# Kernel tuning notes

Hardware: AMD Instinct MI355X
Metric: run time of the kernel (lower is better)

Reference implementation:

```python
import jax, jax.numpy as jnp
import numpy as np

D_MODEL = 1024
N_OCTAVES = 3


def _index_maps(d_model: int, n_octaves: int):
    """Static octave index maps, matching HarmonicMixing._build_index_maps."""
    maps = []
    for octave in range(1, n_octaves + 1):
        stride = 2 ** octave
        up_src = np.arange(d_model // stride)
        up_tgt = up_src * stride                      # i -> i*stride
        down_src = np.arange(stride, d_model)
        down_tgt = down_src // stride                 # i -> i // stride (many-to-one)
        maps.append((up_src, up_tgt, down_src, down_tgt))
    return maps


def setup_inputs() -> dict:
    key = jax.random.key(0)
    k1, k2, k3 = jax.random.split(key, 3)
    x = jax.random.normal(k1, (8, 4096, D_MODEL), dtype=jnp.float32)
    up_weights = jax.random.uniform(k2, (N_OCTAVES,), dtype=jnp.float32)
    down_weights = jax.random.uniform(k3, (N_OCTAVES,), dtype=jnp.float32)
    return {"x": x, "up_weights": up_weights, "down_weights": down_weights}


def reference(x, up_weights, down_weights):
    d_model = x.shape[-1]
    maps = _index_maps(d_model, N_OCTAVES)
    out = x
    for o, (up_src, up_tgt, down_src, down_tgt) in enumerate(maps):
        up_w = jax.nn.sigmoid(up_weights[o])
        down_w = jax.nn.sigmoid(down_weights[o])
        # gather -> scale -> scatter-add (duplicate targets accumulate)
        out = out.at[..., up_tgt].add(up_w * x[..., up_src])
        out = out.at[..., down_tgt].add(down_w * x[..., down_src])
    return out
```

## Files before the change

### kernel.cpp

```cpp
#include <hip/hip_runtime.h>


constexpr int D = 1024;

using f4 = __attribute__((ext_vector_type(4))) float;

__global__ __launch_bounds__(256, 7) void harmonic_kernel(
    const float* __restrict__ x,
    const float* __restrict__ uwp,
    const float* __restrict__ dwp,
    float* __restrict__ out,
    const int n_rows)
{
    __shared__ float rowlo[4][512];
    __shared__ float S1lds[4][512];
    __shared__ float S2lds[4][256];

    const int t = threadIdx.x;
    const int w = t >> 6;
    const int l = t & 63;

    const float uw0 = 1.f / (1.f + __expf(-uwp[0]));
    const float uw1 = 1.f / (1.f + __expf(-uwp[1]));
    const float uw2 = 1.f / (1.f + __expf(-uwp[2]));
    const float dw0 = 1.f / (1.f + __expf(-dwp[0]));
    const float dw1 = 1.f / (1.f + __expf(-dwp[1]));
    const float dw2 = 1.f / (1.f + __expf(-dwp[2]));

    float* const RL = rowlo[w];
    float* const P1 = S1lds[w];
    float* const P2 = S2lds[w];

    auto loadrow = [&](f4* v, const float* p) {
#pragma unroll
        for (int m = 0; m < 4; ++m)
            v[m] = __builtin_nontemporal_load(reinterpret_cast<const f4*>(p + 256 * m));
    };

    auto process = [&](f4* v, float* po) {
        *reinterpret_cast<f4*>(&RL[4 * l])       = v[0];
        *reinterpret_cast<f4*>(&RL[256 + 4 * l]) = v[1];
#pragma unroll
        for (int m = 0; m < 4; ++m) {
            const float s1a = v[m].x + v[m].y;
            const float s1b = v[m].z + v[m].w;
            *reinterpret_cast<float2*>(&P1[128 * m + 2 * l]) = make_float2(s1a, s1b);
            P2[64 * m + l] = s1a + s1b;
        }

#pragma unroll
        for (int m = 0; m < 4; ++m) {
            const float2 u = *reinterpret_cast<const float2*>(&RL[128 * m + 2 * l]);
            v[m].x += uw0 * u.x;
            v[m].z += uw0 * u.y;
            v[m].x += uw1 * RL[64 * m + l];
            if ((l & 1) == 0) v[m].x += uw2 * RL[32 * m + (l >> 1)];
        }

#pragma unroll
        for (int m = 0; m < 2; ++m) {
            const f4 a = *reinterpret_cast<const f4*>(&P1[256 * m + 4 * l]);
            if (m > 0 || l > 0) v[m].x += dw0 * a.x;
            v[m].y += dw0 * a.y;
            v[m].z += dw0 * a.z;
            v[m].w += dw0 * a.w;
        }
        {
            const f4 b = *reinterpret_cast<const f4*>(&P2[4 * l]);
            if (l > 0) v[0].x += dw1 * b.x;
            v[0].y += dw1 * b.y;
            v[0].z += dw1 * b.z;
            v[0].w += dw1 * b.w;
        }
        if (l < 32) {
            const f4 p = *reinterpret_cast<const f4*>(&P2[8 * l]);
            const f4 q = *reinterpret_cast<const f4*>(&P2[8 * l + 4]);
            if (l > 0) v[0].x += dw2 * (p.x + p.y);
            v[0].y += dw2 * (p.z + p.w);
            v[0].z += dw2 * (q.x + q.y);
            v[0].w += dw2 * (q.z + q.w);
        }

#pragma unroll
        for (int m = 0; m < 4; ++m)
            __builtin_nontemporal_store(v[m], reinterpret_cast<f4*>(po + 256 * m));
    };

    const long long rowstep = 4LL * gridDim.x;
    long long row = 4LL * blockIdx.x + w;
    if (row >= n_rows) return;

    f4 vA[4], vB[4];
    loadrow(vA, x + row * D + 4 * l);
    for (;;) {
        const long long rowB = row + rowstep;
        const bool hasB = rowB < n_rows;
        if (hasB) loadrow(vB, x + rowB * D + 4 * l);
        process(vA, out + row * D + 4 * l);
        if (!hasB) return;

        const long long rowC = rowB + rowstep;
        const bool hasC = rowC < n_rows;
        if (hasC) loadrow(vA, x + rowC * D + 4 * l);
        process(vB, out + rowB * D + 4 * l);
        if (!hasC) return;
        row = rowC;
    }
}

extern "C" void kernel_launch(void* const* d_in, const int* in_sizes, int n_in,
                              void* d_out, int out_size, void* d_ws, size_t ws_size,
                              hipStream_t stream) {
    const float* x   = (const float*)d_in[0];
    const float* uwp = (const float*)d_in[1];
    const float* dwp = (const float*)d_in[2];
    float* out = (float*)d_out;
    const int n_rows = in_sizes[0] / D;
    int ngroups = (n_rows + 3) / 4;
    int nb = ngroups < 1792 ? ngroups : 1792;
    harmonic_kernel<<<nb, 256, 0, stream>>>(x, uwp, dwp, out, n_rows);
}
```

Measured before the change: 243.6 us.

## Replace persistent double-buffered grid-stride loop with one-row-per-wave launch

Drops the persistent kernel that software-pipelined row loads across a grid-stride loop and launches one block per four rows, so each wave handles exactly one row. This removes the loop overhead and the extra registers needed for the two row buffers, and relies on hardware wave scheduling to overlap memory latency instead of explicit prefetch. The cost is many more blocks (8192 for the test shape), each recomputing the six sigmoid weights and paying block launch overhead.

```diff
diff --git a/kernel.cpp b/kernel.cpp
--- a/kernel.cpp
+++ b/kernel.cpp
@@ -5,7 +5,7 @@
 
 using f4 = __attribute__((ext_vector_type(4))) float;
 
-__global__ __launch_bounds__(256, 7) void harmonic_kernel(
+__global__ __launch_bounds__(256) void harmonic_kernel(
     const float* __restrict__ x,
     const float* __restrict__ uwp,
     const float* __restrict__ dwp,
@@ -20,6 +20,9 @@
     const int w = t >> 6;
     const int l = t & 63;
 
+    const long long row = 4LL * blockIdx.x + w;
+    if (row >= n_rows) return;
+
     const float uw0 = 1.f / (1.f + __expf(-uwp[0]));
     const float uw1 = 1.f / (1.f + __expf(-uwp[1]));
     const float uw2 = 1.f / (1.f + __expf(-uwp[2]));
@@ -31,81 +34,60 @@
     float* const P1 = S1lds[w];
     float* const P2 = S2lds[w];
 
-    auto loadrow = [&](f4* v, const float* p) {
+    const float* px = x + row * D + 4 * l;
+    float*       po = out + row * D + 4 * l;
+
+    f4 v[4];
 #pragma unroll
-        for (int m = 0; m < 4; ++m)
-            v[m] = __builtin_nontemporal_load(reinterpret_cast<const f4*>(p + 256 * m));
-    };
+    for (int m = 0; m < 4; ++m)
+        v[m] = __builtin_nontemporal_load(reinterpret_cast<const f4*>(px + 256 * m));
 
-    auto process = [&](f4* v, float* po) {
-        *reinterpret_cast<f4*>(&RL[4 * l])       = v[0];
-        *reinterpret_cast<f4*>(&RL[256 + 4 * l]) = v[1];
+    *reinterpret_cast<f4*>(&RL[4 * l])       = v[0];
+    *reinterpret_cast<f4*>(&RL[256 + 4 * l]) = v[1];
 #pragma unroll
-        for (int m = 0; m < 4; ++m) {
-            const float s1a = v[m].x + v[m].y;
-            const float s1b = v[m].z + v[m].w;
-            *reinterpret_cast<float2*>(&P1[128 * m + 2 * l]) = make_float2(s1a, s1b);
-            P2[64 * m + l] = s1a + s1b;
-        }
+    for (int m = 0; m < 4; ++m) {
+        const float s1a = v[m].x + v[m].y;
+        const float s1b = v[m].z + v[m].w;
+        *reinterpret_cast<float2*>(&P1[128 * m + 2 * l]) = make_float2(s1a, s1b);
+        P2[64 * m + l] = s1a + s1b;
+    }
 
 #pragma unroll
-        for (int m = 0; m < 4; ++m) {
-            const float2 u = *reinterpret_cast<const float2*>(&RL[128 * m + 2 * l]);
-            v[m].x += uw0 * u.x;
-            v[m].z += uw0 * u.y;
-            v[m].x += uw1 * RL[64 * m + l];
-            if ((l & 1) == 0) v[m].x += uw2 * RL[32 * m + (l >> 1)];
-        }
+    for (int m = 0; m < 4; ++m) {
+        const float2 u = *reinterpret_cast<const float2*>(&RL[128 * m + 2 * l]);
+        v[m].x += uw0 * u.x;
+        v[m].z += uw0 * u.y;
+        v[m].x += uw1 * RL[64 * m + l];
+        if ((l & 1) == 0) v[m].x += uw2 * RL[32 * m + (l >> 1)];
+    }
 
 #pragma unroll
-        for (int m = 0; m < 2; ++m) {
-            const f4 a = *reinterpret_cast<const f4*>(&P1[256 * m + 4 * l]);
-            if (m > 0 || l > 0) v[m].x += dw0 * a.x;
-            v[m].y += dw0 * a.y;
-            v[m].z += dw0 * a.z;
-            v[m].w += dw0 * a.w;
-        }
-        {
-            const f4 b = *reinterpret_cast<const f4*>(&P2[4 * l]);
-            if (l > 0) v[0].x += dw1 * b.x;
-            v[0].y += dw1 * b.y;
-            v[0].z += dw1 * b.z;
-            v[0].w += dw1 * b.w;
-        }
-        if (l < 32) {
-            const f4 p = *reinterpret_cast<const f4*>(&P2[8 * l]);
-            const f4 q = *reinterpret_cast<const f4*>(&P2[8 * l + 4]);
-            if (l > 0) v[0].x += dw2 * (p.x + p.y);
-            v[0].y += dw2 * (p.z + p.w);
-            v[0].z += dw2 * (q.x + q.y);
-            v[0].w += dw2 * (q.z + q.w);
-        }
+    for (int m = 0; m < 2; ++m) {
+        const f4 a = *reinterpret_cast<const f4*>(&P1[256 * m + 4 * l]);
+        if (m > 0 || l > 0) v[m].x += dw0 * a.x;
+        v[m].y += dw0 * a.y;
+        v[m].z += dw0 * a.z;
+        v[m].w += dw0 * a.w;
+    }
+    {
+        const f4 b = *reinterpret_cast<const f4*>(&P2[4 * l]);
+        if (l > 0) v[0].x += dw1 * b.x;
+        v[0].y += dw1 * b.y;
+        v[0].z += dw1 * b.z;
+        v[0].w += dw1 * b.w;
+    }
+    if (l < 32) {
+        const f4 p = *reinterpret_cast<const f4*>(&P2[8 * l]);
+        const f4 q = *reinterpret_cast<const f4*>(&P2[8 * l + 4]);
+        if (l > 0) v[0].x += dw2 * (p.x + p.y);
+        v[0].y += dw2 * (p.z + p.w);
+        v[0].z += dw2 * (q.x + q.y);
+        v[0].w += dw2 * (q.z + q.w);
+    }
 
 #pragma unroll
-        for (int m = 0; m < 4; ++m)
-            __builtin_nontemporal_store(v[m], reinterpret_cast<f4*>(po + 256 * m));
-    };
-
-    const long long rowstep = 4LL * gridDim.x;
-    long long row = 4LL * blockIdx.x + w;
-    if (row >= n_rows) return;
-
-    f4 vA[4], vB[4];
-    loadrow(vA, x + row * D + 4 * l);
-    for (;;) {
-        const long long rowB = row + rowstep;
-        const bool hasB = rowB < n_rows;
-        if (hasB) loadrow(vB, x + rowB * D + 4 * l);
-        process(vA, out + row * D + 4 * l);
-        if (!hasB) return;
-
-        const long long rowC = rowB + rowstep;
-        const bool hasC = rowC < n_rows;
-        if (hasC) loadrow(vA, x + rowC * D + 4 * l);
-        process(vB, out + rowB * D + 4 * l);
-        if (!hasC) return;
-        row = rowC;
-    }
+    for (int m = 0; m < 4; ++m)
+        __builtin_nontemporal_store(v[m], reinterpret_cast<f4*>(po + 256 * m));
 }
 
 extern "C" void kernel_launch(void* const* d_in, const int* in_sizes, int n_in,
@@ -116,7 +98,6 @@
     const float* dwp = (const float*)d_in[2];
     float* out = (float*)d_out;
     const int n_rows = in_sizes[0] / D;
-    int ngroups = (n_rows + 3) / 4;
-    int nb = ngroups < 1792 ? ngroups : 1792;
+    const int nb = (n_rows + 3) / 4;
     harmonic_kernel<<<nb, 256, 0, stream>>>(x, uwp, dwp, out, n_rows);
 }
```

After: 222.3 us. -8.7%, faster.
